# Optimization experiments

Hardware: AMD Instinct MI355X
Metric: run time of the kernel (lower is better)

Reference implementation:

```python
import jax, jax.numpy as jnp
import numpy as np

B, S, I, H, L, C = 64, 512, 256, 512, 2, 10  # batch, seq, input, hidden, layers, classes

def setup_inputs() -> dict:
    key = jax.random.key(0)
    ks = jax.random.split(key, 12)
    bound = 1.0 / np.sqrt(H)
    u = lambda k, shp: jax.random.uniform(k, shp, jnp.float32, -bound, bound)
    return {
        "x": jax.random.normal(ks[0], (B, S, I), jnp.float32),
        "w_ih0": u(ks[1], (H, I)),  "w_hh0": u(ks[2], (H, H)),
        "b_ih0": u(ks[3], (H,)),    "b_hh0": u(ks[4], (H,)),
        "w_ih1": u(ks[5], (H, H)),  "w_hh1": u(ks[6], (H, H)),
        "b_ih1": u(ks[7], (H,)),    "b_hh1": u(ks[8], (H,)),
        "w_fc": u(ks[9], (C, H)),   "b_fc": u(ks[10], (C,)),
    }

def _rnn_layer(x_seq, w_ih, w_hh, b_ih, b_hh):
    # Precompute input projection for all timesteps as one big GEMM.
    pre = jnp.einsum('bsi,hi->bsh', x_seq, w_ih) + b_ih + b_hh  # (B,S,H)
    def step(h, p_t):
        h = jnp.tanh(p_t + h @ w_hh.T)
        return h, h
    h0 = jnp.zeros((x_seq.shape[0], w_hh.shape[0]), x_seq.dtype)
    h_last, ys = jax.lax.scan(step, h0, jnp.swapaxes(pre, 0, 1))  # scan over time
    return jnp.swapaxes(ys, 0, 1), h_last  # (B,S,H), (B,H)

def reference(x, w_ih0, w_hh0, b_ih0, b_hh0, w_ih1, w_hh1, b_ih1, b_hh1, w_fc, b_fc):
    out0, _ = _rnn_layer(x, w_ih0, w_hh0, b_ih0, b_hh0)
    _, h_last = _rnn_layer(out0, w_ih1, w_hh1, b_ih1, b_hh1)
    # classification head: final hidden of top layer -> (dropout p=0) -> linear
    return h_last @ w_fc.T + b_fc  # (B, C)
```

## Files before the change

kernel.cpp:

```cpp
#include <hip/hip_runtime.h>
#include <hip/hip_bf16.h>
#include <math.h>


typedef __attribute__((ext_vector_type(8))) short  short8;
typedef __attribute__((ext_vector_type(4))) float  floatx4;
typedef __attribute__((ext_vector_type(4))) unsigned int uintx4;

#define MFMA_BF16(a, b, c) __builtin_amdgcn_mfma_f32_16x16x32_bf16((a), (b), (c), 0, 0, 0)

#define OFS_HH0   ((size_t)0)
#define OFS_HH1   ((size_t)262144)
#define OFS_IH1   ((size_t)524288)
#define OFS_IH0   ((size_t)786432)
#define OFS_XB    ((size_t)1048576)
#define HEX_BYTE   ((size_t)1835008)
#define FLAGS_BYTE ((size_t)18874368)
#define PRE_B      ((size_t)52428800)

__device__ __forceinline__ unsigned short f2bf(float f) {
    unsigned u = __builtin_bit_cast(unsigned, f);
    u += 0x7fffu + ((u >> 16) & 1u);
    return (unsigned short)(u >> 16);
}
__device__ __forceinline__ float bf2f(unsigned short h) {
    return __builtin_bit_cast(float, ((unsigned)h) << 16);
}
__device__ __forceinline__ float fast_tanh(float x) {
    float z = fminf(9.0f, fmaxf(-9.0f, x));
    float e = __builtin_amdgcn_exp2f(z * 2.88539008f);
    return (e - 1.0f) * __builtin_amdgcn_rcpf(e + 1.0f);
}
__device__ __forceinline__ void inv_l1() {
    asm volatile("buffer_inv sc0" ::: "memory");
}

__device__ __forceinline__ void pack_w(const float* __restrict__ W,
                                       unsigned short* __restrict__ Wp,
                                       int KT, int idx) {
    int l  = idx & 63;
    int kt = (idx >> 6) % KT;
    int nt = (idx >> 6) / KT;
    int Kdim = KT * 32;
    int row = nt * 16 + (l & 15);
    int col = kt * 32 + (l >> 4) * 8;
    const float* s = W + (size_t)row * Kdim + col;
    short8 v;
#pragma unroll
    for (int j = 0; j < 8; ++j) v[j] = (short)f2bf(s[j]);
    *(short8*)(Wp + (size_t)idx * 8) = v;
}

__global__ void prep_kernel(const float* __restrict__ x,
                            const float* __restrict__ whh0,
                            const float* __restrict__ whh1,
                            const float* __restrict__ wih1,
                            const float* __restrict__ wih0,
                            unsigned short* __restrict__ wsb) {
    int blk = blockIdx.x, tid = threadIdx.x;
    if (blk < 128) {
        pack_w(whh0, wsb + OFS_HH0, 16, blk * 256 + tid);
    } else if (blk < 256) {
        pack_w(whh1, wsb + OFS_HH1, 16, (blk - 128) * 256 + tid);
    } else if (blk < 384) {
        pack_w(wih1, wsb + OFS_IH1, 16, (blk - 256) * 256 + tid);
    } else if (blk < 448) {
        pack_w(wih0, wsb + OFS_IH0, 8, (blk - 384) * 256 + tid);
    } else if (blk < 4544) {
        size_t e = ((size_t)(blk - 448) * 256 + tid) * 8;
        const float* s = x + e;
        short8 v;
#pragma unroll
        for (int j = 0; j < 8; ++j) v[j] = (short)f2bf(s[j]);
        *(short8*)(wsb + OFS_XB + e) = v;
    } else {
        ((unsigned int*)((char*)wsb + FLAGS_BYTE))[tid] = 0u;
    }
}

__global__ __launch_bounds__(512) void proj_kernel(
        const unsigned short* __restrict__ A,
        const unsigned short* __restrict__ Wp,
        const float* __restrict__ bias1, const float* __restrict__ bias2,
        float* __restrict__ out, int KT) {
    int tid = threadIdx.x, blk = blockIdx.x;
    int w = tid >> 6, l = tid & 63, lm = l & 15, lq = l >> 4;
    int mg = w >> 1, nh = w & 1;
    int Kdim = KT * 32;
    int r0 = blk * 64 + mg * 16;

    floatx4 acc[16];
#pragma unroll
    for (int i = 0; i < 16; ++i) acc[i] = (floatx4)0.f;

    for (int kt = 0; kt < KT; ++kt) {
        short8 a = *(const short8*)(A + (size_t)(r0 + lm) * Kdim + kt * 32 + lq * 8);
#pragma unroll
        for (int i = 0; i < 16; ++i) {
            int ntg = nh * 16 + i;
            short8 b = *(const short8*)(Wp + (((size_t)ntg * KT + kt) * 64 + l) * 8);
            acc[i] = MFMA_BF16(a, b, acc[i]);
        }
    }
#pragma unroll
    for (int i = 0; i < 16; ++i) {
        int n = (nh * 16 + i) * 16 + lm;
        float bs = bias1[n] + bias2[n];
        int slice2 = n >> 6, w2 = (n >> 4) & 3, lm2 = n & 15;
#pragma unroll
        for (int r = 0; r < 4; ++r) {
            int row = r0 + lq * 4 + r;
            int b = row >> 9, tt = row & 511;
            int g2 = b >> 4, br = b & 15;
            int lblk2 = g2 * 8 + slice2;
            int tid2 = w2 * 64 + (br >> 2) * 16 + lm2;
            size_t idx = (((size_t)tt * 32 + lblk2) * 256 + tid2) * 4 + (br & 3);
            out[idx] = acc[i][r] + bs;
        }
    }
}

__global__ __launch_bounds__(512, 2) void fused_kernel(
        const float* __restrict__ pre,
        const unsigned short* __restrict__ Whh0,
        const unsigned short* __restrict__ Whh1,
        const unsigned short* __restrict__ Wih1,
        unsigned int* __restrict__ hex,
        unsigned int* __restrict__ flags,
        const float* __restrict__ bih1, const float* __restrict__ bhh1,
        const float* __restrict__ wfc, const float* __restrict__ bfc,
        float* __restrict__ out) {
    const int pblk = blockIdx.x;
    if ((pblk & 7) >= 4) return;

    __shared__ unsigned short h0[2][16][512];
    __shared__ unsigned short h1[2][16][512];
    __shared__ float red0[256][5];
    __shared__ float red1[256][5];

    const int tid = threadIdx.x;
    const int w = tid >> 6, l = tid & 63, lm = l & 15, lq = l >> 4;
    const int wk = w >> 2, wn = w & 3;
    const int g = pblk & 7, slice = pblk >> 3;
    const int lblk = g * 8 + slice;
    const int ntg = slice * 4 + wn;
    const int ncol = ntg * 16 + lm;
    const int s2 = slice * 2;
    const int rid = tid & 255;

    {
        uintx4* z0 = (uintx4*)&h0[0][0][0];
        uintx4* z1 = (uintx4*)&h1[0][0][0];
        for (int i = tid; i < 1024; i += 512) { z0[i] = (uintx4)0u; z1[i] = (uintx4)0u; }
    }
    short8 WA[8], WB[8], WC[8];
#pragma unroll
    for (int j = 0; j < 8; ++j) {
        int kt = (s2 + wk * 8 + j) & 15;
        size_t src = (((size_t)ntg * 16 + kt) * 64 + l) * 8;
        WA[j] = *(const short8*)(Whh0 + src);
        WB[j] = *(const short8*)(Wih1 + src);
        WC[j] = *(const short8*)(Whh1 + src);
        asm volatile("" : "+a"(WA[j]), "+a"(WB[j]), "+a"(WC[j]));
    }
    const float b1v = bih1[ncol] + bhh1[ncol];

    const int cch = tid & 63;
    const int rbase = tid >> 6;
    const bool dl = (cch >> 3) != slice;
    const bool poller = (w == 1) && (l < 7);
    const int ps = (slice + 1 + l) & 7;
    const int mychunk = ncol >> 3;

    __syncthreads();

    for (int i = 0; i <= 512; ++i) {
        const int sl = i & 1, slw = sl ^ 1;

        if (poller && i >= 1) {
            unsigned int tgt = (unsigned int)i;
            while (__hip_atomic_load(&flags[g * 8 + ps],
                                     __ATOMIC_RELAXED, __HIP_MEMORY_SCOPE_AGENT) < tgt)
                ;
        }
        __syncthreads();
        inv_l1();

        const bool ld0 = dl && (i >= 1);
        const bool ld1 = dl && (i >= 2);
        uintx4 v00, v01, v10, v11;
        if (ld0) {
            const uintx4* s = (const uintx4*)(hex + (size_t)((sl * 4 + g) * 2 + 0) * 4096);
            v00 = s[rbase * 64 + cch];
            v01 = s[(rbase + 8) * 64 + cch];
        }
        if (ld1) {
            const uintx4* s = (const uintx4*)(hex + (size_t)((sl * 4 + g) * 2 + 1) * 4096);
            v10 = s[rbase * 64 + cch];
            v11 = s[(rbase + 8) * 64 + cch];
        }
        floatx4 pv = (floatx4)0.f;
        if (wk == 0 && i <= 511)
            pv = *(const floatx4*)(pre + (((size_t)i * 32 + lblk) * 256 + tid) * 4);

        floatx4 acc0p = (floatx4)0.f, accA = (floatx4)0.f, accB = (floatx4)0.f;
        if (wk == 0) {
#pragma unroll
            for (int j = 0; j < 2; ++j) {
                int kt = s2 + j;
                int ch = ((kt * 4 + lq) ^ (lm & 7)) << 3;
                short8 a = *(const short8*)&h0[sl][lm][ch];
                acc0p = MFMA_BF16(a, WA[j], acc0p);
                accA  = MFMA_BF16(a, WB[j], accA);
                short8 a1 = *(const short8*)&h1[sl][lm][ch];
                accB  = MFMA_BF16(a1, WC[j], accB);
            }
        }

        if (ld0) {
            int r0r = rbase, r1r = rbase + 8;
            *(uintx4*)&h0[sl][r0r][(cch ^ (r0r & 7)) * 8] = v00;
            *(uintx4*)&h0[sl][r1r][(cch ^ (r1r & 7)) * 8] = v01;
        }
        if (ld1) {
            int r0r = rbase, r1r = rbase + 8;
            *(uintx4*)&h1[sl][r0r][(cch ^ (r0r & 7)) * 8] = v10;
            *(uintx4*)&h1[sl][r1r][(cch ^ (r1r & 7)) * 8] = v11;
        }
        __syncthreads();

        if (wk == 0) {
#pragma unroll
            for (int j = 2; j < 8; ++j) {
                int kt = (s2 + j) & 15;
                int ch = ((kt * 4 + lq) ^ (lm & 7)) << 3;
                short8 a = *(const short8*)&h0[sl][lm][ch];
                acc0p = MFMA_BF16(a, WA[j], acc0p);
                accA  = MFMA_BF16(a, WB[j], accA);
                short8 a1 = *(const short8*)&h1[sl][lm][ch];
                accB  = MFMA_BF16(a1, WC[j], accB);
            }
        } else {
#pragma unroll
            for (int j = 0; j < 8; ++j) {
                int kt = (s2 + 8 + j) & 15;
                int ch = ((kt * 4 + lq) ^ (lm & 7)) << 3;
                short8 a = *(const short8*)&h0[sl][lm][ch];
                acc0p = MFMA_BF16(a, WA[j], acc0p);
                accA  = MFMA_BF16(a, WB[j], accA);
                short8 a1 = *(const short8*)&h1[sl][lm][ch];
                accB  = MFMA_BF16(a1, WC[j], accB);
            }
        }

        if (wk == 0) {
#pragma unroll
            for (int r = 0; r < 4; ++r) red1[rid][r] = accA[r] + accB[r];
        } else {
#pragma unroll
            for (int r = 0; r < 4; ++r) red0[rid][r] = acc0p[r];
        }
        __syncthreads();

        if (wk == 0 && i <= 511) {
            unsigned int* exw = hex + (size_t)((slw * 4 + g) * 2 + 0) * 4096;
#pragma unroll
            for (int r = 0; r < 4; ++r) {
                int row = lq * 4 + r;
                unsigned int hb = f2bf(fast_tanh(acc0p[r] + red0[rid][r] + pv[r]));
                unsigned int pk = hb | ((unsigned int)__shfl_xor((int)hb, 1) << 16);
                if (!(lm & 1)) {
                    *(unsigned int*)&h0[slw][row][((mychunk ^ (row & 7)) << 3) | (ncol & 7)] = pk;
                    exw[(size_t)row * 256 + (ncol >> 1)] = pk;
                }
            }
        }
        if (wk == 1 && i >= 1) {
            unsigned int* exw = hex + (size_t)((slw * 4 + g) * 2 + 1) * 4096;
#pragma unroll
            for (int r = 0; r < 4; ++r) {
                int row = lq * 4 + r;
                unsigned int hb =
                    f2bf(fast_tanh(accA[r] + accB[r] + red1[rid][r] + b1v));
                unsigned int pk = hb | ((unsigned int)__shfl_xor((int)hb, 1) << 16);
                if (!(lm & 1)) {
                    *(unsigned int*)&h1[slw][row][((mychunk ^ (row & 7)) << 3) | (ncol & 7)] = pk;
                    exw[(size_t)row * 256 + (ncol >> 1)] = pk;
                }
            }
        }

        __syncthreads();

        if (tid == 0)
            __hip_atomic_store(&flags[lblk], (unsigned int)(i + 1),
                               __ATOMIC_RELAXED, __HIP_MEMORY_SCOPE_AGENT);
    }

    if (slice == 0) {
        if (poller) {
            while (__hip_atomic_load(&flags[g * 8 + ps],
                                     __ATOMIC_RELAXED, __HIP_MEMORY_SCOPE_AGENT) < 513u)
                ;
        }
        __syncthreads();
        inv_l1();
        if (dl) {
            const uintx4* s = (const uintx4*)(hex + (size_t)((1 * 4 + g) * 2 + 1) * 4096);
            uintx4 a = s[rbase * 64 + cch];
            uintx4 b = s[(rbase + 8) * 64 + cch];
            int r0r = rbase, r1r = rbase + 8;
            *(uintx4*)&h1[1][r0r][(cch ^ (r0r & 7)) * 8] = a;
            *(uintx4*)&h1[1][r1r][(cch ^ (r1r & 7)) * 8] = b;
        }
        __syncthreads();
        if (tid < 160) {
            int b = tid / 10, c = tid % 10;
            float s = bfc[c];
            for (int n = 0; n < 512; ++n) {
                unsigned short hb = h1[1][b][(((n >> 3) ^ (b & 7)) << 3) | (n & 7)];
                s += bf2f(hb) * wfc[c * 512 + n];
            }
            out[(size_t)(g * 16 + b) * 10 + c] = s;
        }
    }
}

extern "C" void kernel_launch(void* const* d_in, const int* in_sizes, int n_in,
                              void* d_out, int out_size, void* d_ws, size_t ws_size,
                              hipStream_t stream) {
    const float* x    = (const float*)d_in[0];
    const float* wih0 = (const float*)d_in[1];
    const float* whh0 = (const float*)d_in[2];
    const float* bih0 = (const float*)d_in[3];
    const float* bhh0 = (const float*)d_in[4];
    const float* wih1 = (const float*)d_in[5];
    const float* whh1 = (const float*)d_in[6];
    const float* bih1 = (const float*)d_in[7];
    const float* bhh1 = (const float*)d_in[8];
    const float* wfc  = (const float*)d_in[9];
    const float* bfc  = (const float*)d_in[10];
    float* out = (float*)d_out;

    unsigned short* wsb  = (unsigned short*)d_ws;
    unsigned short* xb   = wsb + OFS_XB;
    unsigned int* hex    = (unsigned int*)((char*)d_ws + HEX_BYTE);
    unsigned int* flags  = (unsigned int*)((char*)d_ws + FLAGS_BYTE);
    float* pre = (float*)((char*)d_ws + PRE_B);

    prep_kernel<<<dim3(4545), dim3(256), 0, stream>>>(x, whh0, whh1, wih1, wih0, wsb);
    proj_kernel<<<dim3(512), dim3(512), 0, stream>>>(xb, wsb + OFS_IH0, bih0, bhh0, pre, 8);
    fused_kernel<<<dim3(60), dim3(512), 0, stream>>>(
        pre, wsb + OFS_HH0, wsb + OFS_HH1, wsb + OFS_IH1,
        hex, flags, bih1, bhh1, wfc, bfc, out);
}
```

Measured before the change: 1.388 ms.

## Split recurrent K-reduction across 16 waves with 1024-thread blocks

Doubles the fused recurrent kernel's block size to 1024 threads so each wave handles 4 K-tiles instead of 8. Partial sums from the extra waves go through enlarged LDS reduction buffers. The layer-1 accumulators are merged into one, and each thread loads one hex row instead of two. This shortens the serial MFMA chain per timestep, at the cost of more cross-wave reduction traffic and heavier barriers on the latency-critical step loop.

```diff
diff --git a/kernel.cpp b/kernel.cpp
--- a/kernel.cpp
+++ b/kernel.cpp
@@ -120,7 +120,7 @@
     }
 }
 
-__global__ __launch_bounds__(512, 2) void fused_kernel(
+__global__ __launch_bounds__(1024, 1) void fused_kernel(
         const float* __restrict__ pre,
         const unsigned short* __restrict__ Whh0,
         const unsigned short* __restrict__ Whh1,
@@ -135,8 +135,8 @@
 
     __shared__ unsigned short h0[2][16][512];
     __shared__ unsigned short h1[2][16][512];
-    __shared__ float red0[256][5];
-    __shared__ float red1[256][5];
+    __shared__ float red0[3][256][5];
+    __shared__ float red1[3][256][5];
 
     const int tid = threadIdx.x;
     const int w = tid >> 6, l = tid & 63, lm = l & 15, lq = l >> 4;
@@ -151,12 +151,12 @@
     {
         uintx4* z0 = (uintx4*)&h0[0][0][0];
         uintx4* z1 = (uintx4*)&h1[0][0][0];
-        for (int i = tid; i < 1024; i += 512) { z0[i] = (uintx4)0u; z1[i] = (uintx4)0u; }
-    }
-    short8 WA[8], WB[8], WC[8];
-#pragma unroll
-    for (int j = 0; j < 8; ++j) {
-        int kt = (s2 + wk * 8 + j) & 15;
+        for (int i = tid; i < 2048; i += 1024) { z0[i] = (uintx4)0u; z1[i] = (uintx4)0u; }
+    }
+    short8 WA[4], WB[4], WC[4];
+#pragma unroll
+    for (int j = 0; j < 4; ++j) {
+        int kt = (s2 + wk * 4 + j) & 15;
         size_t src = (((size_t)ntg * 16 + kt) * 64 + l) * 8;
         WA[j] = *(const short8*)(Whh0 + src);
         WB[j] = *(const short8*)(Wih1 + src);
@@ -166,7 +166,7 @@
     const float b1v = bih1[ncol] + bhh1[ncol];
 
     const int cch = tid & 63;
-    const int rbase = tid >> 6;
+    const int rquad = tid >> 6;
     const bool dl = (cch >> 3) != slice;
     const bool poller = (w == 1) && (l < 7);
     const int ps = (slice + 1 + l) & 7;
@@ -188,22 +188,18 @@
 
         const bool ld0 = dl && (i >= 1);
         const bool ld1 = dl && (i >= 2);
-        uintx4 v00, v01, v10, v11;
-        if (ld0) {
-            const uintx4* s = (const uintx4*)(hex + (size_t)((sl * 4 + g) * 2 + 0) * 4096);
-            v00 = s[rbase * 64 + cch];
-            v01 = s[(rbase + 8) * 64 + cch];
-        }
-        if (ld1) {
-            const uintx4* s = (const uintx4*)(hex + (size_t)((sl * 4 + g) * 2 + 1) * 4096);
-            v10 = s[rbase * 64 + cch];
-            v11 = s[(rbase + 8) * 64 + cch];
-        }
+        uintx4 v0, v1;
+        if (ld0)
+            v0 = ((const uintx4*)(hex + (size_t)((sl * 4 + g) * 2 + 0) * 4096))
+                     [rquad * 64 + cch];
+        if (ld1)
+            v1 = ((const uintx4*)(hex + (size_t)((sl * 4 + g) * 2 + 1) * 4096))
+                     [rquad * 64 + cch];
         floatx4 pv = (floatx4)0.f;
         if (wk == 0 && i <= 511)
             pv = *(const floatx4*)(pre + (((size_t)i * 32 + lblk) * 256 + tid) * 4);
 
-        floatx4 acc0p = (floatx4)0.f, accA = (floatx4)0.f, accB = (floatx4)0.f;
+        floatx4 acc0p = (floatx4)0.f, acc1p = (floatx4)0.f;
         if (wk == 0) {
 #pragma unroll
             for (int j = 0; j < 2; ++j) {
@@ -211,54 +207,48 @@
                 int ch = ((kt * 4 + lq) ^ (lm & 7)) << 3;
                 short8 a = *(const short8*)&h0[sl][lm][ch];
                 acc0p = MFMA_BF16(a, WA[j], acc0p);
-                accA  = MFMA_BF16(a, WB[j], accA);
+                acc1p = MFMA_BF16(a, WB[j], acc1p);
                 short8 a1 = *(const short8*)&h1[sl][lm][ch];
-                accB  = MFMA_BF16(a1, WC[j], accB);
-            }
-        }
-
-        if (ld0) {
-            int r0r = rbase, r1r = rbase + 8;
-            *(uintx4*)&h0[sl][r0r][(cch ^ (r0r & 7)) * 8] = v00;
-            *(uintx4*)&h0[sl][r1r][(cch ^ (r1r & 7)) * 8] = v01;
-        }
-        if (ld1) {
-            int r0r = rbase, r1r = rbase + 8;
-            *(uintx4*)&h1[sl][r0r][(cch ^ (r0r & 7)) * 8] = v10;
-            *(uintx4*)&h1[sl][r1r][(cch ^ (r1r & 7)) * 8] = v11;
-        }
+                acc1p = MFMA_BF16(a1, WC[j], acc1p);
+            }
+        }
+
+        if (ld0) *(uintx4*)&h0[sl][rquad][(cch ^ (rquad & 7)) * 8] = v0;
+        if (ld1) *(uintx4*)&h1[sl][rquad][(cch ^ (rquad & 7)) * 8] = v1;
         __syncthreads();
 
         if (wk == 0) {
 #pragma unroll
-            for (int j = 2; j < 8; ++j) {
+            for (int j = 2; j < 4; ++j) {
                 int kt = (s2 + j) & 15;
                 int ch = ((kt * 4 + lq) ^ (lm & 7)) << 3;
                 short8 a = *(const short8*)&h0[sl][lm][ch];
                 acc0p = MFMA_BF16(a, WA[j], acc0p);
-                accA  = MFMA_BF16(a, WB[j], accA);
+                acc1p = MFMA_BF16(a, WB[j], acc1p);
                 short8 a1 = *(const short8*)&h1[sl][lm][ch];
-                accB  = MFMA_BF16(a1, WC[j], accB);
+                acc1p = MFMA_BF16(a1, WC[j], acc1p);
             }
         } else {
 #pragma unroll
-            for (int j = 0; j < 8; ++j) {
-                int kt = (s2 + 8 + j) & 15;
+            for (int j = 0; j < 4; ++j) {
+                int kt = (s2 + wk * 4 + j) & 15;
                 int ch = ((kt * 4 + lq) ^ (lm & 7)) << 3;
                 short8 a = *(const short8*)&h0[sl][lm][ch];
                 acc0p = MFMA_BF16(a, WA[j], acc0p);
-                accA  = MFMA_BF16(a, WB[j], accA);
+                acc1p = MFMA_BF16(a, WB[j], acc1p);
                 short8 a1 = *(const short8*)&h1[sl][lm][ch];
-                accB  = MFMA_BF16(a1, WC[j], accB);
-            }
-        }
-
-        if (wk == 0) {
-#pragma unroll
-            for (int r = 0; r < 4; ++r) red1[rid][r] = accA[r] + accB[r];
-        } else {
-#pragma unroll
-            for (int r = 0; r < 4; ++r) red0[rid][r] = acc0p[r];
+                acc1p = MFMA_BF16(a1, WC[j], acc1p);
+            }
+        }
+
+        if (wk != 0) {
+#pragma unroll
+            for (int r = 0; r < 4; ++r) red0[wk - 1][rid][r] = acc0p[r];
+        }
+        if (wk != 1) {
+            int ridx = (wk == 0) ? 0 : wk - 1;
+#pragma unroll
+            for (int r = 0; r < 4; ++r) red1[ridx][rid][r] = acc1p[r];
         }
         __syncthreads();
 
@@ -267,7 +257,9 @@
 #pragma unroll
             for (int r = 0; r < 4; ++r) {
                 int row = lq * 4 + r;
-                unsigned int hb = f2bf(fast_tanh(acc0p[r] + red0[rid][r] + pv[r]));
+                float v = acc0p[r] + red0[0][rid][r] + red0[1][rid][r]
+                          + red0[2][rid][r] + pv[r];
+                unsigned int hb = f2bf(fast_tanh(v));
                 unsigned int pk = hb | ((unsigned int)__shfl_xor((int)hb, 1) << 16);
                 if (!(lm & 1)) {
                     *(unsigned int*)&h0[slw][row][((mychunk ^ (row & 7)) << 3) | (ncol & 7)] = pk;
@@ -280,8 +272,9 @@
 #pragma unroll
             for (int r = 0; r < 4; ++r) {
                 int row = lq * 4 + r;
-                unsigned int hb =
-                    f2bf(fast_tanh(accA[r] + accB[r] + red1[rid][r] + b1v));
+                float v = acc1p[r] + red1[0][rid][r] + red1[1][rid][r]
+                          + red1[2][rid][r] + b1v;
+                unsigned int hb = f2bf(fast_tanh(v));
                 unsigned int pk = hb | ((unsigned int)__shfl_xor((int)hb, 1) << 16);
                 if (!(lm & 1)) {
                     *(unsigned int*)&h1[slw][row][((mychunk ^ (row & 7)) << 3) | (ncol & 7)] = pk;
@@ -306,12 +299,9 @@
         __syncthreads();
         inv_l1();
         if (dl) {
-            const uintx4* s = (const uintx4*)(hex + (size_t)((1 * 4 + g) * 2 + 1) * 4096);
-            uintx4 a = s[rbase * 64 + cch];
-            uintx4 b = s[(rbase + 8) * 64 + cch];
-            int r0r = rbase, r1r = rbase + 8;
-            *(uintx4*)&h1[1][r0r][(cch ^ (r0r & 7)) * 8] = a;
-            *(uintx4*)&h1[1][r1r][(cch ^ (r1r & 7)) * 8] = b;
+            uintx4 v = ((const uintx4*)(hex + (size_t)((1 * 4 + g) * 2 + 1) * 4096))
+                           [rquad * 64 + cch];
+            *(uintx4*)&h1[1][rquad][(cch ^ (rquad & 7)) * 8] = v;
         }
         __syncthreads();
         if (tid < 160) {
@@ -350,7 +340,7 @@
 
     prep_kernel<<<dim3(4545), dim3(256), 0, stream>>>(x, whh0, whh1, wih1, wih0, wsb);
     proj_kernel<<<dim3(512), dim3(512), 0, stream>>>(xb, wsb + OFS_IH0, bih0, bhh0, pre, 8);
-    fused_kernel<<<dim3(60), dim3(512), 0, stream>>>(
+    fused_kernel<<<dim3(60), dim3(1024), 0, stream>>>(
         pre, wsb + OFS_HH0, wsb + OFS_HH1, wsb + OFS_IH1,
         hex, flags, bih1, bhh1, wfc, bfc, out);
 }
```

Measured after the change: 1.827 ms. +31.6%, slower.
